# Performance work log

Measured on AMD Instinct MI355X. Metric: run time of the kernel, lower is better.

Reference implementation:

```python
import jax, jax.numpy as jnp
import numpy as np

B, T, C, H, WIN = 1, 2048, 512, 8, 48
DH = C // H  # 64


def setup_inputs() -> dict:
    key = jax.random.key(0)
    kx, kq, ko, kp = jax.random.split(key, 4)
    x = jax.random.normal(kx, (B, T, C), dtype=jnp.float32)
    W_qkv = jax.random.normal(kq, (C, 3 * C), dtype=jnp.float32) / np.sqrt(C).astype(np.float32)
    W_out = jax.random.normal(ko, (C, C), dtype=jnp.float32) / np.sqrt(C).astype(np.float32)
    # one random cycle permutation per head: perms[h, pi_pos] = original_pos
    perms = jax.vmap(lambda k: jax.random.permutation(k, T))(jax.random.split(kp, H)).astype(jnp.int32)
    return {"x": x, "W_qkv": W_qkv, "W_out": W_out, "perms": perms}


def _head_attn(qh, kh, vh, perm):
    # qh, kh, vh: [B, T, DH]; perm: [T] with perm[pi_pos] = original_pos
    Tn = perm.shape[0]
    inv_perm = jnp.argsort(perm)  # inv_perm[orig_pos] = pi_pos
    q_pi = qh[:, perm]
    k_pi = kh[:, perm]
    v_pi = vh[:, perm]
    offs = jnp.arange(-WIN, WIN + 1)                      # [W]
    pi_idx = jnp.arange(Tn)[:, None] + offs[None, :]      # [T, W]
    idx = jnp.clip(pi_idx, 0, Tn - 1)
    k_win = k_pi[:, idx]                                  # [B, T, W, DH]
    v_win = v_pi[:, idx]                                  # [B, T, W, DH]
    scores = jnp.einsum('btd,btwd->btw', q_pi, k_win) / np.sqrt(DH).astype(np.float32)
    neigh_orig = perm[idx]                                # [T, W] original positions of neighbors
    mask = (neigh_orig <= perm[:, None]) & (pi_idx >= 0) & (pi_idx < Tn)  # causal + window validity
    scores = jnp.where(mask[None], scores, jnp.finfo(scores.dtype).min)
    w = jax.nn.softmax(scores, axis=-1)                   # [B, T, W]
    y_pi = jnp.einsum('btw,btwd->btd', w, v_win)          # [B, T, DH]
    return y_pi[:, inv_perm]                              # back to original order


def reference(x, W_qkv, W_out, perms):
    qkv = x @ W_qkv                                       # [B, T, 3C]
    q, k, v = jnp.split(qkv, 3, axis=-1)
    q = q.reshape(B, T, H, DH)
    k = k.reshape(B, T, H, DH)
    v = v.reshape(B, T, H, DH)
    # heads are independent; vmap over head axis with per-head permutation
    y = jax.vmap(_head_attn, in_axes=(2, 2, 2, 0), out_axes=2)(q, k, v, perms)  # [B, T, H, DH]
    return y.reshape(B, T, C) @ W_out
```

## Files before the change

### kernel.cpp

```cpp
#include <hip/hip_runtime.h>
#include <float.h>
#include <math.h>

#define T_DIM 2048
#define C_DIM 512
#define QKV_LD 1536
#define NBLK 512

typedef float f32x4 __attribute__((ext_vector_type(4)));
typedef short s16x8 __attribute__((ext_vector_type(8)));

__device__ __forceinline__ unsigned short f2bf(float f) {
  unsigned u = __float_as_uint(f);
  return (unsigned short)((u + 0x7fffu + ((u >> 16) & 1u)) >> 16);
}

__device__ __forceinline__ void load16_to_lds(const void* g, void* l) {
  __builtin_amdgcn_global_load_lds(
      (const __attribute__((address_space(1))) unsigned int*)g,
      (__attribute__((address_space(3))) unsigned int*)(unsigned int)(unsigned long long)l,
      16, 0, 0);
}

__global__ __launch_bounds__(256) void prep_kernel(const float* __restrict__ x,
                                                   const float* __restrict__ Wqkv,
                                                   const float* __restrict__ Wout,
                                                   unsigned short* __restrict__ xbf,
                                                   unsigned short* __restrict__ WqkvT,
                                                   unsigned short* __restrict__ WoutT) {
  __shared__ float tile[32][33];
  const int tid = threadIdx.x, bid = blockIdx.x;

  const float4* xs4 = (const float4*)x;
  for (int i = bid * 256 + tid; i < (T_DIM * C_DIM) / 4; i += NBLK * 256) {
    float4 v = xs4[i];
    ushort4 o;
    o.x = f2bf(v.x); o.y = f2bf(v.y); o.z = f2bf(v.z); o.w = f2bf(v.w);
    ((ushort4*)xbf)[i] = o;
  }
  const int tx = tid & 31, ty = tid >> 5;
  for (int tt = bid; tt < 1024; tt += NBLK) {
    const float* src; unsigned short* dst; int Cc, R, bx, by;
    if (tt < 768) { src = Wqkv; dst = WqkvT; Cc = QKV_LD; R = C_DIM; bx = (tt % 48) * 32; by = (tt / 48) * 32; }
    else { int u = tt - 768; src = Wout; dst = WoutT; Cc = C_DIM; R = C_DIM; bx = (u & 15) * 32; by = (u >> 4) * 32; }
    __syncthreads();
#pragma unroll
    for (int i = 0; i < 4; ++i) { int r = ty + i * 8; tile[r][tx] = src[(size_t)(by + r) * Cc + bx + tx]; }
    __syncthreads();
#pragma unroll
    for (int i = 0; i < 4; ++i) { int r = ty + i * 8; dst[(size_t)(bx + r) * R + by + tx] = f2bf(tile[tx][r]); }
  }
}

template <int BM, int BN, bool OUT16>
__device__ __forceinline__ void gemm_body(const unsigned short* __restrict__ A,
                                          const unsigned short* __restrict__ BT,
                                          void* __restrict__ Cp,
                                          int N, int K, int tilesX,
                                          unsigned short* lA, unsigned short* lB,
                                          int tid, int bid) {
  constexpr int BK = 32;
  constexpr int ASZ = BM * BK, BSZ = BN * BK;
  constexpr int BM2 = BM / 2, BN2 = BN / 2;
  constexpr int MT = BM2 / 16, NT = BN2 / 16;
  constexpr int IA = BM / 64;
  constexpr int IB = BN / 64;
  const int lane = tid & 63, w = tid >> 6, wr = w >> 1, wc = w & 1;
  const int fm = lane & 15, q8 = (lane >> 4) * 8, q4 = lane >> 4;

  const int m0 = (bid / tilesX) * BM, n0 = (bid % tilesX) * BN;

  auto stage = [&](int t, int buf) {
    const int k0 = t * BK;
    unsigned short* dA = lA + buf * ASZ;
    unsigned short* dB = lB + buf * BSZ;
#pragma unroll
    for (int i = 0; i < IA; ++i) {
      int c = i * 256 + tid, row = c >> 2, c8 = (c & 3) * 8;
      load16_to_lds(&A[(size_t)(m0 + row) * K + k0 + c8], dA + c * 8);
    }
#pragma unroll
    for (int i = 0; i < IB; ++i) {
      int c = i * 256 + tid, row = c >> 2, c8 = (c & 3) * 8;
      load16_to_lds(&BT[(size_t)(n0 + row) * K + k0 + c8], dB + c * 8);
    }
  };

  f32x4 acc[MT][NT] = {};
  const int nt = K / BK;
  stage(0, 0);
  for (int t = 0; t < nt; ++t) {
    const int cur = t & 1;
    __syncthreads();
    if (t + 1 < nt) stage(t + 1, cur ^ 1);
    const unsigned short* sA = lA + cur * ASZ;
    const unsigned short* sB = lB + cur * BSZ;
    s16x8 a[MT], b[NT];
#pragma unroll
    for (int mi = 0; mi < MT; ++mi)
      a[mi] = *(const s16x8*)&sA[(wr * BM2 + mi * 16 + fm) * BK + q8];
#pragma unroll
    for (int ni = 0; ni < NT; ++ni)
      b[ni] = *(const s16x8*)&sB[(wc * BN2 + ni * 16 + fm) * BK + q8];
#pragma unroll
    for (int mi = 0; mi < MT; ++mi)
#pragma unroll
      for (int ni = 0; ni < NT; ++ni)
        acc[mi][ni] = __builtin_amdgcn_mfma_f32_16x16x32_bf16(a[mi], b[ni], acc[mi][ni], 0, 0, 0);
  }
#pragma unroll
  for (int mi = 0; mi < MT; ++mi)
#pragma unroll
    for (int ni = 0; ni < NT; ++ni)
#pragma unroll
      for (int r = 0; r < 4; ++r) {
        int row = m0 + wr * BM2 + mi * 16 + q4 * 4 + r;
        int col = n0 + wc * BN2 + ni * 16 + fm;
        if constexpr (OUT16)
          ((unsigned short*)Cp)[(size_t)row * N + col] = f2bf(acc[mi][ni][r]);
        else
          ((float*)Cp)[(size_t)row * N + col] = acc[mi][ni][r];
      }
}

__global__ __launch_bounds__(256) void gemm1_kernel(const unsigned short* __restrict__ A,
                                                    const unsigned short* __restrict__ BT,
                                                    unsigned short* __restrict__ Cc) {
  __shared__ __align__(16) unsigned short smem[2 * (128 + 128) * 32];
  gemm_body<128, 128, true>(A, BT, Cc, QKV_LD, C_DIM, 12, smem, smem + 2 * 128 * 32,
                            threadIdx.x, blockIdx.x);
}
__global__ __launch_bounds__(256) void gemm2_kernel(const unsigned short* __restrict__ A,
                                                    const unsigned short* __restrict__ BT,
                                                    float* __restrict__ Cc) {
  __shared__ __align__(16) unsigned short smem[2 * (64 + 64) * 32];
  gemm_body<64, 64, false>(A, BT, Cc, C_DIM, C_DIM, 8, smem, smem + 2 * 64 * 32,
                           threadIdx.x, blockIdx.x);
}

__global__ __launch_bounds__(256) void attn_kernel(const unsigned short* __restrict__ qkvbf,
                                                   const int* __restrict__ perms,
                                                   unsigned short* __restrict__ Ybf) {
  __shared__ __align__(16) unsigned char smem[48768];
  int* ow            = (int*)smem;
  unsigned short* lQ = (unsigned short*)(smem + 512);
  unsigned short* lK = (unsigned short*)(smem + 5120);
  float* Sb          = (float*)(smem + 23552);
  unsigned short* lP = (unsigned short*)(smem + 40064);
  unsigned short* lVT= (unsigned short*)(smem + 5120);

  const int tid = threadIdx.x, bid = blockIdx.x;
  const int lane = tid & 63, w = tid >> 6;
  const int fm = lane & 15, q8 = (lane >> 4) * 8, q4 = lane >> 4;
  const int h = bid >> 6;
  const int t0 = (bid & 63) << 5;

  if (tid < 128) {
    int pi = t0 - 48 + tid;
    int idx = min(max(pi, 0), T_DIM - 1);
    ow[tid] = perms[h * T_DIM + idx];
  }
  __syncthreads();

#pragma unroll
  for (int it = 0; it < 4; ++it) {
    int c = it * 256 + tid;
    int row = c >> 3, k8 = c & 7;
    uint4 d = *(const uint4*)(qkvbf + (size_t)ow[row] * QKV_LD + C_DIM + h * 64 + k8 * 8);
    *(uint4*)(lK + row * 72 + k8 * 8) = d;
  }
  {
    int row = tid >> 3, k8 = tid & 7;
    uint4 d = *(const uint4*)(qkvbf + (size_t)ow[48 + row] * QKV_LD + h * 64 + k8 * 8);
    *(uint4*)(lQ + row * 72 + k8 * 8) = d;
  }

  uint4 va[2], vb[2];
#pragma unroll
  for (int it = 0; it < 2; ++it) {
    int c2 = it * 256 + tid;
    int r = c2 & 63, d0 = (c2 >> 6) * 8;
    va[it] = *(const uint4*)(qkvbf + (size_t)ow[2 * r]     * QKV_LD + 2 * C_DIM + h * 64 + d0);
    vb[it] = *(const uint4*)(qkvbf + (size_t)ow[2 * r + 1] * QKV_LD + 2 * C_DIM + h * 64 + d0);
  }
  __syncthreads();

  {
    f32x4 accs[2][2] = {};
#pragma unroll
    for (int kt = 0; kt < 2; ++kt) {
      s16x8 aq[2];
#pragma unroll
      for (int mi = 0; mi < 2; ++mi)
        aq[mi] = *(const s16x8*)&lQ[(mi * 16 + fm) * 72 + kt * 32 + q8];
#pragma unroll
      for (int ni = 0; ni < 2; ++ni) {
        s16x8 bk = *(const s16x8*)&lK[(w * 32 + ni * 16 + fm) * 72 + kt * 32 + q8];
#pragma unroll
        for (int mi = 0; mi < 2; ++mi)
          accs[mi][ni] = __builtin_amdgcn_mfma_f32_16x16x32_bf16(aq[mi], bk, accs[mi][ni], 0, 0, 0);
      }
    }
#pragma unroll
    for (int mi = 0; mi < 2; ++mi)
#pragma unroll
      for (int ni = 0; ni < 2; ++ni)
#pragma unroll
        for (int r = 0; r < 4; ++r)
          Sb[(mi * 16 + q4 * 4 + r) * 129 + w * 32 + ni * 16 + fm] = accs[mi][ni][r] * 0.125f;
  }
  __syncthreads();

#pragma unroll
  for (int it = 0; it < 2; ++it) {
    int c2 = it * 256 + tid;
    int r = c2 & 63, d0 = (c2 >> 6) * 8;
    uint4 a4 = va[it], b4 = vb[it];
    *(unsigned*)(lVT + (d0 + 0) * 136 + 2 * r) = (a4.x & 0xffffu) | (b4.x << 16);
    *(unsigned*)(lVT + (d0 + 1) * 136 + 2 * r) = (a4.x >> 16) | (b4.x & 0xffff0000u);
    *(unsigned*)(lVT + (d0 + 2) * 136 + 2 * r) = (a4.y & 0xffffu) | (b4.y << 16);
    *(unsigned*)(lVT + (d0 + 3) * 136 + 2 * r) = (a4.y >> 16) | (b4.y & 0xffff0000u);
    *(unsigned*)(lVT + (d0 + 4) * 136 + 2 * r) = (a4.z & 0xffffu) | (b4.z << 16);
    *(unsigned*)(lVT + (d0 + 5) * 136 + 2 * r) = (a4.z >> 16) | (b4.z & 0xffff0000u);
    *(unsigned*)(lVT + (d0 + 6) * 136 + 2 * r) = (a4.w & 0xffffu) | (b4.w << 16);
    *(unsigned*)(lVT + (d0 + 7) * 136 + 2 * r) = (a4.w >> 16) | (b4.w & 0xffff0000u);
  }

  for (int si = 0; si < 8; ++si) {
    const int s = w * 8 + si;
    const int p = ow[48 + s];
    const int c1 = lane + 64;
    const float v0 = Sb[s * 129 + lane];
    const float v1 = Sb[s * 129 + c1];
    const int pi0 = t0 - 48 + lane;
    const bool valid0 = (lane >= s) && (pi0 >= 0) && (pi0 < T_DIM) && (ow[lane] <= p);
    const bool valid1 = (lane <= s + 32) && (pi0 + 64 < T_DIM) && (ow[c1] <= p);
    float mx = fmaxf(valid0 ? v0 : -FLT_MAX, valid1 ? v1 : -FLT_MAX);
#pragma unroll
    for (int off = 32; off > 0; off >>= 1) mx = fmaxf(mx, __shfl_xor(mx, off, 64));
    const float e0 = valid0 ? __expf(v0 - mx) : 0.f;
    const float e1 = valid1 ? __expf(v1 - mx) : 0.f;
    float sum = e0 + e1;
#pragma unroll
    for (int off = 32; off > 0; off >>= 1) sum += __shfl_xor(sum, off, 64);
    const float inv = 1.f / sum;
    lP[s * 136 + lane] = valid0 ? f2bf(e0 * inv) : (unsigned short)0;
    lP[s * 136 + c1]   = valid1 ? f2bf(e1 * inv) : (unsigned short)0;
  }
  __syncthreads();

  {
    const int wr = w >> 1, wc = w & 1;
    f32x4 acco[2] = {};
#pragma unroll
    for (int kt = 0; kt < 4; ++kt) {
      s16x8 ap = *(const s16x8*)&lP[(wr * 16 + fm) * 136 + kt * 32 + q8];
#pragma unroll
      for (int ni = 0; ni < 2; ++ni) {
        s16x8 bv = *(const s16x8*)&lVT[((wc * 2 + ni) * 16 + fm) * 136 + kt * 32 + q8];
        acco[ni] = __builtin_amdgcn_mfma_f32_16x16x32_bf16(ap, bv, acco[ni], 0, 0, 0);
      }
    }
#pragma unroll
    for (int ni = 0; ni < 2; ++ni)
#pragma unroll
      for (int r = 0; r < 4; ++r) {
        int q = wr * 16 + q4 * 4 + r;
        int d = (wc * 2 + ni) * 16 + fm;
        Ybf[(size_t)ow[48 + q] * C_DIM + h * 64 + d] = f2bf(acco[ni][r]);
      }
  }
}

extern "C" void kernel_launch(void* const* d_in, const int* in_sizes, int n_in,
                              void* d_out, int out_size, void* d_ws, size_t ws_size,
                              hipStream_t stream) {
  const float* x     = (const float*)d_in[0];
  const float* Wqkv  = (const float*)d_in[1];
  const float* Wout  = (const float*)d_in[2];
  const int*   perms = (const int*)d_in[3];
  float* out = (float*)d_out;
  unsigned short* ws = (unsigned short*)d_ws;

  unsigned short* xbf   = ws;
  unsigned short* WqkvT = xbf + 1048576;
  unsigned short* WoutT = WqkvT + 786432;
  unsigned short* qkvbf = WoutT + 262144;
  unsigned short* Ybf   = qkvbf + 3145728;

  prep_kernel<<<NBLK, 256, 0, stream>>>(x, Wqkv, Wout, xbf, WqkvT, WoutT);
  gemm1_kernel<<<192, 256, 0, stream>>>(xbf, WqkvT, qkvbf);
  attn_kernel<<<NBLK, 256, 0, stream>>>(qkvbf, perms, Ybf);
  gemm2_kernel<<<256, 256, 0, stream>>>(Ybf, WoutT, out);
}
```

Baseline: 93.29 us.

## Fuse fp32-to-bf16 casts and weight transpose into GEMM staging, drop prep kernel

```diff
diff --git a/kernel.cpp b/kernel.cpp
--- a/kernel.cpp
+++ b/kernel.cpp
@@ -9,6 +9,7 @@
 
 typedef float f32x4 __attribute__((ext_vector_type(4)));
 typedef short s16x8 __attribute__((ext_vector_type(8)));
+typedef unsigned u32x4 __attribute__((ext_vector_type(4)));
 
 __device__ __forceinline__ unsigned short f2bf(float f) {
   unsigned u = __float_as_uint(f);
@@ -22,86 +23,111 @@
       16, 0, 0);
 }
 
-__global__ __launch_bounds__(256) void prep_kernel(const float* __restrict__ x,
-                                                   const float* __restrict__ Wqkv,
-                                                   const float* __restrict__ Wout,
-                                                   unsigned short* __restrict__ xbf,
-                                                   unsigned short* __restrict__ WqkvT,
-                                                   unsigned short* __restrict__ WoutT) {
-  __shared__ float tile[32][33];
-  const int tid = threadIdx.x, bid = blockIdx.x;
-
-  const float4* xs4 = (const float4*)x;
-  for (int i = bid * 256 + tid; i < (T_DIM * C_DIM) / 4; i += NBLK * 256) {
-    float4 v = xs4[i];
-    ushort4 o;
-    o.x = f2bf(v.x); o.y = f2bf(v.y); o.z = f2bf(v.z); o.w = f2bf(v.w);
-    ((ushort4*)xbf)[i] = o;
-  }
-  const int tx = tid & 31, ty = tid >> 5;
-  for (int tt = bid; tt < 1024; tt += NBLK) {
-    const float* src; unsigned short* dst; int Cc, R, bx, by;
-    if (tt < 768) { src = Wqkv; dst = WqkvT; Cc = QKV_LD; R = C_DIM; bx = (tt % 48) * 32; by = (tt / 48) * 32; }
-    else { int u = tt - 768; src = Wout; dst = WoutT; Cc = C_DIM; R = C_DIM; bx = (u & 15) * 32; by = (u >> 4) * 32; }
-    __syncthreads();
-#pragma unroll
-    for (int i = 0; i < 4; ++i) { int r = ty + i * 8; tile[r][tx] = src[(size_t)(by + r) * Cc + bx + tx]; }
-    __syncthreads();
-#pragma unroll
-    for (int i = 0; i < 4; ++i) { int r = ty + i * 8; dst[(size_t)(bx + r) * R + by + tx] = f2bf(tile[tx][r]); }
-  }
-}
-
-template <int BM, int BN, bool OUT16>
-__device__ __forceinline__ void gemm_body(const unsigned short* __restrict__ A,
-                                          const unsigned short* __restrict__ BT,
+template <int BM, int BN, int KDIM, bool A_CAST, bool OUT16>
+__device__ __forceinline__ void gemm_body(const void* __restrict__ Ap,
+                                          const float* __restrict__ Bw,
                                           void* __restrict__ Cp,
-                                          int N, int K, int tilesX,
+                                          int N, int ldb, int tilesX,
                                           unsigned short* lA, unsigned short* lB,
                                           int tid, int bid) {
   constexpr int BK = 32;
-  constexpr int ASZ = BM * BK, BSZ = BN * BK;
+  constexpr int LDA = A_CAST ? 40 : 32;
+  constexpr int LDB = 40;
+  constexpr int ASZ = BM * LDA, BSZ = BN * LDB;
+  constexpr int KPT = BN * 16 / 256;
   constexpr int BM2 = BM / 2, BN2 = BN / 2;
   constexpr int MT = BM2 / 16, NT = BN2 / 16;
-  constexpr int IA = BM / 64;
-  constexpr int IB = BN / 64;
+  constexpr int nt = KDIM / BK;
+  static_assert(!A_CAST || BM == 128, "A cast staging assumes BM=128");
+
   const int lane = tid & 63, w = tid >> 6, wr = w >> 1, wc = w & 1;
   const int fm = lane & 15, q8 = (lane >> 4) * 8, q4 = lane >> 4;
-
   const int m0 = (bid / tilesX) * BM, n0 = (bid % tilesX) * BN;
 
-  auto stage = [&](int t, int buf) {
-    const int k0 = t * BK;
-    unsigned short* dA = lA + buf * ASZ;
-    unsigned short* dB = lB + buf * BSZ;
-#pragma unroll
-    for (int i = 0; i < IA; ++i) {
+  const int bn = tid & (BN - 1);
+  const int bkp0 = (tid / BN) * KPT;
+  const float* Bbase = Bw + (size_t)(2 * bkp0) * ldb + n0 + bn;
+  float fb[2 * KPT];
+
+  const float* Af = (const float*)Ap;
+  const unsigned short* Abf = (const unsigned short*)Ap;
+  const int arow = tid >> 1, akh = tid & 1;
+  float fa[16];
+
+  auto loadB = [&](int t) {
+#pragma unroll
+    for (int j = 0; j < 2 * KPT; ++j)
+      fb[j] = Bbase[(size_t)(t * BK + j) * ldb];
+  };
+  auto writeB = [&](unsigned short* dB) {
+    unsigned pk[KPT];
+#pragma unroll
+    for (int pj = 0; pj < KPT; ++pj)
+      pk[pj] = (unsigned)f2bf(fb[2 * pj]) | ((unsigned)f2bf(fb[2 * pj + 1]) << 16);
+#pragma unroll
+    for (int c = 0; c < KPT / 4; ++c) {
+      u32x4 u = {pk[4 * c], pk[4 * c + 1], pk[4 * c + 2], pk[4 * c + 3]};
+      *(u32x4*)(dB + (size_t)bn * LDB + 2 * (bkp0 + 4 * c)) = u;
+    }
+  };
+  auto loadA = [&](int t) {
+    if constexpr (A_CAST) {
+#pragma unroll
+      for (int i = 0; i < 4; ++i) {
+        float4 v = *(const float4*)(Af + (size_t)(m0 + arow) * KDIM + t * BK + akh * 16 + i * 4);
+        fa[4 * i] = v.x; fa[4 * i + 1] = v.y; fa[4 * i + 2] = v.z; fa[4 * i + 3] = v.w;
+      }
+    }
+  };
+  auto writeA = [&](unsigned short* dA) {
+    unsigned pk[8];
+#pragma unroll
+    for (int j = 0; j < 8; ++j)
+      pk[j] = (unsigned)f2bf(fa[2 * j]) | ((unsigned)f2bf(fa[2 * j + 1]) << 16);
+#pragma unroll
+    for (int c = 0; c < 2; ++c) {
+      u32x4 u = {pk[4 * c], pk[4 * c + 1], pk[4 * c + 2], pk[4 * c + 3]};
+      *(u32x4*)(dA + (size_t)arow * LDA + akh * 16 + c * 8) = u;
+    }
+  };
+  auto stageA_lds = [&](int t, unsigned short* dA) {
+#pragma unroll
+    for (int i = 0; i < BM / 64; ++i) {
       int c = i * 256 + tid, row = c >> 2, c8 = (c & 3) * 8;
-      load16_to_lds(&A[(size_t)(m0 + row) * K + k0 + c8], dA + c * 8);
-    }
-#pragma unroll
-    for (int i = 0; i < IB; ++i) {
-      int c = i * 256 + tid, row = c >> 2, c8 = (c & 3) * 8;
-      load16_to_lds(&BT[(size_t)(n0 + row) * K + k0 + c8], dB + c * 8);
-    }
-  };
+      load16_to_lds(&Abf[(size_t)(m0 + row) * KDIM + t * BK + c8], dA + c * 8);
+    }
+  };
+
+  loadB(0);
+  if constexpr (A_CAST) loadA(0); else stageA_lds(0, lA);
+  writeB(lB);
+  if constexpr (A_CAST) writeA(lA);
+  loadB(1);
+  if constexpr (A_CAST) loadA(1);
 
   f32x4 acc[MT][NT] = {};
-  const int nt = K / BK;
-  stage(0, 0);
   for (int t = 0; t < nt; ++t) {
     const int cur = t & 1;
+    unsigned short* cA = lA + cur * ASZ;
+    unsigned short* cB = lB + cur * BSZ;
+    unsigned short* nA = lA + (cur ^ 1) * ASZ;
+    unsigned short* nB = lB + (cur ^ 1) * BSZ;
     __syncthreads();
-    if (t + 1 < nt) stage(t + 1, cur ^ 1);
-    const unsigned short* sA = lA + cur * ASZ;
-    const unsigned short* sB = lB + cur * BSZ;
     s16x8 a[MT], b[NT];
 #pragma unroll
     for (int mi = 0; mi < MT; ++mi)
-      a[mi] = *(const s16x8*)&sA[(wr * BM2 + mi * 16 + fm) * BK + q8];
+      a[mi] = *(const s16x8*)&cA[(size_t)(wr * BM2 + mi * 16 + fm) * LDA + q8];
 #pragma unroll
     for (int ni = 0; ni < NT; ++ni)
-      b[ni] = *(const s16x8*)&sB[(wc * BN2 + ni * 16 + fm) * BK + q8];
+      b[ni] = *(const s16x8*)&cB[(size_t)(wc * BN2 + ni * 16 + fm) * LDB + q8];
+    if (t + 1 < nt) {
+      writeB(nB);
+      if constexpr (A_CAST) writeA(nA); else stageA_lds(t + 1, nA);
+    }
+    if (t + 2 < nt) {
+      loadB(t + 2);
+      if constexpr (A_CAST) loadA(t + 2);
+    }
 #pragma unroll
     for (int mi = 0; mi < MT; ++mi)
 #pragma unroll
@@ -123,19 +149,21 @@
       }
 }
 
-__global__ __launch_bounds__(256) void gemm1_kernel(const unsigned short* __restrict__ A,
-                                                    const unsigned short* __restrict__ BT,
+__global__ __launch_bounds__(256) void gemm1_kernel(const float* __restrict__ x,
+                                                    const float* __restrict__ Wqkv,
                                                     unsigned short* __restrict__ Cc) {
-  __shared__ __align__(16) unsigned short smem[2 * (128 + 128) * 32];
-  gemm_body<128, 128, true>(A, BT, Cc, QKV_LD, C_DIM, 12, smem, smem + 2 * 128 * 32,
-                            threadIdx.x, blockIdx.x);
-}
-__global__ __launch_bounds__(256) void gemm2_kernel(const unsigned short* __restrict__ A,
-                                                    const unsigned short* __restrict__ BT,
+  __shared__ __align__(16) unsigned short smem[2 * 128 * 40 + 2 * 128 * 40];
+  gemm_body<128, 128, C_DIM, true, true>(x, Wqkv, Cc, QKV_LD, QKV_LD, 12,
+                                         smem, smem + 2 * 128 * 40,
+                                         threadIdx.x, blockIdx.x);
+}
+__global__ __launch_bounds__(256) void gemm2_kernel(const unsigned short* __restrict__ Ybf,
+                                                    const float* __restrict__ Wout,
                                                     float* __restrict__ Cc) {
-  __shared__ __align__(16) unsigned short smem[2 * (64 + 64) * 32];
-  gemm_body<64, 64, false>(A, BT, Cc, C_DIM, C_DIM, 8, smem, smem + 2 * 64 * 32,
-                           threadIdx.x, blockIdx.x);
+  __shared__ __align__(16) unsigned short smem[2 * 64 * 32 + 2 * 64 * 40];
+  gemm_body<64, 64, C_DIM, false, false>(Ybf, Wout, Cc, C_DIM, C_DIM, 8,
+                                         smem, smem + 2 * 64 * 32,
+                                         threadIdx.x, blockIdx.x);
 }
 
 __global__ __launch_bounds__(256) void attn_kernel(const unsigned short* __restrict__ qkvbf,
@@ -282,14 +310,10 @@
   float* out = (float*)d_out;
   unsigned short* ws = (unsigned short*)d_ws;
 
-  unsigned short* xbf   = ws;
-  unsigned short* WqkvT = xbf + 1048576;
-  unsigned short* WoutT = WqkvT + 786432;
-  unsigned short* qkvbf = WoutT + 262144;
+  unsigned short* qkvbf = ws;
   unsigned short* Ybf   = qkvbf + 3145728;
 
-  prep_kernel<<<NBLK, 256, 0, stream>>>(x, Wqkv, Wout, xbf, WqkvT, WoutT);
-  gemm1_kernel<<<192, 256, 0, stream>>>(xbf, WqkvT, qkvbf);
+  gemm1_kernel<<<192, 256, 0, stream>>>(x, Wqkv, qkvbf);
   attn_kernel<<<NBLK, 256, 0, stream>>>(qkvbf, perms, Ybf);
-  gemm2_kernel<<<256, 256, 0, stream>>>(Ybf, WoutT, out);
-}
+  gemm2_kernel<<<256, 256, 0, stream>>>(Ybf, Wout, out);
+}
```

Result: slower. 101.1 us (+8.4%).
